# Kernel optimization log

Hardware: AMD Instinct MI355X
Metric: run time of the kernel (lower is better)

## Reference

```python
import jax, jax.numpy as jnp
import numpy as np

N = 10000
F_IN = 512
HID = 256
N_CLS = 64


def setup_inputs() -> dict:
    key = jax.random.key(0)
    k_feat, k_adj, k_w1, k_b1, k_w2, k_b2 = jax.random.split(key, 6)
    feature = jax.random.normal(k_feat, (N, F_IN), dtype=jnp.float32)
    # normalized-adjacency-like dense matrix (sparse-ish values, scaled)
    adj = jax.random.uniform(k_adj, (N, N), dtype=jnp.float32) * (1.0 / N)
    # GCNConv params: glorot-style weights, zero bias
    s1 = 1.0 / np.sqrt(F_IN)
    s2 = 1.0 / np.sqrt(HID)
    W1 = jax.random.uniform(k_w1, (F_IN, HID), jnp.float32, -s1, s1)
    b1 = jnp.zeros((HID,), jnp.float32)
    W2 = jax.random.uniform(k_w2, (HID, N_CLS), jnp.float32, -s2, s2)
    b2 = jnp.zeros((N_CLS,), jnp.float32)
    return {"feature": feature, "adj": adj, "W1": W1, "b1": b1, "W2": W2, "b2": b2}


def gcn_conv(x, adj, W, b):
    # support = x @ W ; out = adj @ support + b
    return adj @ (x @ W) + b


def reference(feature, adj, W1, b1, W2, b2):
    x1 = jax.nn.relu(gcn_conv(feature, adj, W1, b1))
    # dropout is identity in eval mode
    x2 = gcn_conv(x1, adj, W2, b2)
    return (x1, jax.nn.log_softmax(x2, axis=1))
```

## Files before the change

### kernel.cpp

```cpp
#include <hip/hip_runtime.h>
#include <hip/hip_bf16.h>


#define NROW 10000
#define FIN  512
#define HID  256
#define NCLS 64
#define KSPLIT2 4
#define KSPAN2  2560
#define KSPLIT4 8
#define KSPAN4  1280

typedef __bf16 bf8_t __attribute__((ext_vector_type(8)));
typedef __bf16 bf4_t __attribute__((ext_vector_type(4)));
typedef float  f4_t  __attribute__((ext_vector_type(4)));
typedef short  s8_t  __attribute__((ext_vector_type(8)));

__global__ void cvt_f32_bf16(const float* __restrict__ in, __bf16* __restrict__ out, int n) {
    int stride = gridDim.x * blockDim.x * 4;
    for (int i = (blockIdx.x * blockDim.x + threadIdx.x) * 4; i < n; i += stride) {
        f4_t v = *(const f4_t*)(in + i);
        bf4_t o;
        o[0] = (__bf16)v[0]; o[1] = (__bf16)v[1]; o[2] = (__bf16)v[2]; o[3] = (__bf16)v[3];
        *(bf4_t*)(out + i) = o;
    }
}

__global__ void cvt_transpose(const float* __restrict__ in, __bf16* __restrict__ out, int K, int Nn) {
    int idx = blockIdx.x * 256 + threadIdx.x;
    if (idx < K * Nn) {
        int k = idx / Nn, n = idx % Nn;
        out[n * K + k] = (__bf16)in[idx];
    }
}

template<int BM, int BN, int BK, bool AF32, int EPI>
__global__ void __launch_bounds__(256, 4)
gemm_bt(const void* __restrict__ Ap, const __bf16* __restrict__ Bt,
        int M, int Nn, int K, int lda, int ldb, int kspan,
        float* __restrict__ outF, __bf16* __restrict__ outB,
        int ldo, long partStride)
{
    constexpr int WM = BM / 2, WN = BN / 2;
    constexpr int MI = WM / 16, NI = WN / 16;
    constexpr int LDS_K = BK + 8;
    __shared__ __bf16 As[BM * LDS_K];
    __shared__ __bf16 Bs[BN * LDS_K];

    const int tid  = threadIdx.x;
    const int lane = tid & 63;
    const int wave = tid >> 6;
    const int wm = wave >> 1, wn = wave & 1;
    const int m0 = blockIdx.x * BM;
    const int n0 = blockIdx.y * BN;
    const int kbase = blockIdx.z * kspan;
    const int kend  = min(K, kbase + kspan);

    f4_t acc[MI][NI];
    #pragma unroll
    for (int i = 0; i < MI; i++)
        #pragma unroll
        for (int j = 0; j < NI; j++)
            acc[i][j] = f4_t{0.f, 0.f, 0.f, 0.f};

    const int lrow  = lane & 15;
    const int koff0 = (lane >> 4) * 8;

    for (int k0 = kbase; k0 < kend; k0 += BK) {
        if constexpr (AF32) {
            const float* A = (const float*)Ap;
            #pragma unroll
            for (int i = 0; i < BM * BK / 4 / 256; ++i) {
                int idx = tid + i * 256;
                int r = idx / (BK / 4), c = idx % (BK / 4);
                int gm = m0 + r, gk = k0 + c * 4;
                f4_t v = f4_t{0.f, 0.f, 0.f, 0.f};
                if (gm < M && gk < kend) v = *(const f4_t*)(A + (long)gm * lda + gk);
                bf4_t o;
                o[0] = (__bf16)v[0]; o[1] = (__bf16)v[1]; o[2] = (__bf16)v[2]; o[3] = (__bf16)v[3];
                *(bf4_t*)&As[r * LDS_K + c * 4] = o;
            }
        } else {
            const short* A = (const short*)Ap;
            #pragma unroll
            for (int i = 0; i < BM * BK / 8 / 256; ++i) {
                int idx = tid + i * 256;
                int r = idx / (BK / 8), c = idx % (BK / 8);
                int gm = m0 + r, gk = k0 + c * 8;
                s8_t v = s8_t{0,0,0,0,0,0,0,0};
                if (gm < M && gk < kend) v = *(const s8_t*)(A + (long)gm * lda + gk);
                *(s8_t*)&As[r * LDS_K + c * 8] = v;
            }
        }
        {
            const short* B = (const short*)Bt;
            #pragma unroll
            for (int i = 0; i < BN * BK / 8 / 256; ++i) {
                int idx = tid + i * 256;
                int r = idx / (BK / 8), c = idx % (BK / 8);
                int gn = n0 + r, gk = k0 + c * 8;
                s8_t v = s8_t{0,0,0,0,0,0,0,0};
                if (gn < Nn && gk < kend) v = *(const s8_t*)(B + (long)gn * ldb + gk);
                *(s8_t*)&Bs[r * LDS_K + c * 8] = v;
            }
        }
        __syncthreads();
        #pragma unroll
        for (int ks = 0; ks < BK; ks += 32) {
            bf8_t af[MI], bfv[NI];
            #pragma unroll
            for (int mi = 0; mi < MI; mi++)
                af[mi] = *(const bf8_t*)&As[(wm * WM + mi * 16 + lrow) * LDS_K + ks + koff0];
            #pragma unroll
            for (int ni = 0; ni < NI; ni++)
                bfv[ni] = *(const bf8_t*)&Bs[(wn * WN + ni * 16 + lrow) * LDS_K + ks + koff0];
            #pragma unroll
            for (int mi = 0; mi < MI; mi++)
                #pragma unroll
                for (int ni = 0; ni < NI; ni++)
                    acc[mi][ni] = __builtin_amdgcn_mfma_f32_16x16x32_bf16(
                        af[mi], bfv[ni], acc[mi][ni], 0, 0, 0);
        }
        __syncthreads();
    }

    const int erow = wm * WM + (lane >> 4) * 4;
    const int ecol = wn * WN + lrow;
    #pragma unroll
    for (int mi = 0; mi < MI; mi++) {
        #pragma unroll
        for (int ni = 0; ni < NI; ni++) {
            #pragma unroll
            for (int r = 0; r < 4; r++) {
                int grow = m0 + erow + mi * 16 + r;
                int gcol = n0 + ecol + ni * 16;
                if (grow < M && gcol < Nn) {
                    float v = acc[mi][ni][r];
                    if constexpr (EPI == 0) {
                        outB[(long)grow * ldo + gcol] = (__bf16)v;
                    } else {
                        outF[blockIdx.z * partStride + (long)grow * ldo + gcol] = v;
                    }
                }
            }
        }
    }
}

__global__ void relu_bias_fin(const float* __restrict__ part, const float* __restrict__ b1,
                              float* __restrict__ outF, __bf16* __restrict__ outB) {
    long i = (long)(blockIdx.x * 256 + threadIdx.x) * 4;
    f4_t v = *(const f4_t*)(part + i);
    #pragma unroll
    for (int s = 1; s < KSPLIT2; s++) {
        f4_t p = *(const f4_t*)(part + (long)s * NROW * HID + i);
        v[0] += p[0]; v[1] += p[1]; v[2] += p[2]; v[3] += p[3];
    }
    int col = (int)(i & (HID - 1));
    f4_t b = *(const f4_t*)(b1 + col);
    f4_t y;
    bf4_t yb;
    #pragma unroll
    for (int j = 0; j < 4; j++) {
        y[j] = fmaxf(v[j] + b[j], 0.f);
        yb[j] = (__bf16)y[j];
    }
    *(f4_t*)(outF + i) = y;
    *(bf4_t*)(outB + i) = yb;
}

__global__ void logsoftmax_fin(const float* __restrict__ part, const float* __restrict__ b2,
                               float* __restrict__ out, int M) {
    int row  = blockIdx.x * 4 + (threadIdx.x >> 6);
    int lane = threadIdx.x & 63;
    if (row >= M) return;
    float v = b2[lane];
    #pragma unroll
    for (int s = 0; s < KSPLIT4; s++) v += part[((long)s * M + row) * NCLS + lane];
    float m = v;
    #pragma unroll
    for (int off = 32; off > 0; off >>= 1) m = fmaxf(m, __shfl_xor(m, off));
    float e = __expf(v - m);
    float sum = e;
    #pragma unroll
    for (int off = 32; off > 0; off >>= 1) sum += __shfl_xor(sum, off);
    out[(long)row * NCLS + lane] = (v - m) - __logf(sum);
}

extern "C" void kernel_launch(void* const* d_in, const int* in_sizes, int n_in,
                              void* d_out, int out_size, void* d_ws, size_t ws_size,
                              hipStream_t stream) {
    const float* feat = (const float*)d_in[0];
    const float* adj  = (const float*)d_in[1];
    const float* W1   = (const float*)d_in[2];
    const float* b1   = (const float*)d_in[3];
    const float* W2   = (const float*)d_in[4];
    const float* b2   = (const float*)d_in[5];
    float* out = (float*)d_out;
    char* ws = (char*)d_ws;

    __bf16* featb = (__bf16*)(ws);
    __bf16* W1t   = (__bf16*)(ws + 10240000);
    __bf16* W2t   = (__bf16*)(ws + 10502144);
    __bf16* S1t   = (__bf16*)(ws + 10534912);
    __bf16* x1b   = (__bf16*)(ws + 15654912);
    __bf16* S2t   = (__bf16*)(ws + 20774912);
    float*  part  = (float*) (ws + 22054912);

    cvt_f32_bf16<<<640, 256, 0, stream>>>(feat, featb, NROW * FIN);
    cvt_transpose<<<(FIN * HID + 255) / 256, 256, 0, stream>>>(W1, W1t, FIN, HID);
    cvt_transpose<<<(HID * NCLS + 255) / 256, 256, 0, stream>>>(W2, W2t, HID, NCLS);

    gemm_bt<64, 128, 64, false, 0><<<dim3(4, 79, 1), 256, 0, stream>>>(
        W1t, featb, HID, NROW, FIN, FIN, FIN, FIN,
        nullptr, S1t, NROW, 0);

    gemm_bt<64, 128, 64, true, 2><<<dim3(157, 2, KSPLIT2), 256, 0, stream>>>(
        adj, S1t, NROW, HID, NROW, NROW, NROW, KSPAN2,
        part, nullptr, HID, (long)NROW * HID);

    relu_bias_fin<<<NROW * HID / 4 / 256, 256, 0, stream>>>(part, b1, out, x1b);

    gemm_bt<64, 64, 64, false, 0><<<dim3(1, 157, 1), 256, 0, stream>>>(
        W2t, x1b, NCLS, NROW, HID, HID, HID, HID,
        nullptr, S2t, NROW, 0);

    gemm_bt<64, 64, 64, true, 2><<<dim3(157, 1, KSPLIT4), 256, 0, stream>>>(
        adj, S2t, NROW, NCLS, NROW, NROW, NROW, KSPAN4,
        part, nullptr, NCLS, (long)NROW * NCLS);

    logsoftmax_fin<<<2500, 256, 0, stream>>>(part, b2, out + (long)NROW * HID, NROW);
}
```

Before: 886.3 us.

## Prefetch next K-tile into registers while computing current tile in GEMM

Restructures the GEMM main loop so global loads for the next K-tile are issued into registers before the MFMA compute on the current LDS tile. The loaded values are written to LDS at the start of the next iteration. This hides global memory latency behind compute in a software-pipelined way, at the cost of extra registers that may reduce occupancy under the 256x4 launch bounds.

```diff
diff --git a/kernel.cpp b/kernel.cpp
--- a/kernel.cpp
+++ b/kernel.cpp
@@ -44,6 +44,8 @@
     constexpr int WM = BM / 2, WN = BN / 2;
     constexpr int MI = WM / 16, NI = WN / 16;
     constexpr int LDS_K = BK + 8;
+    constexpr int ACH = AF32 ? (BM * BK / 4 / 256) : (BM * BK / 8 / 256);
+    constexpr int BCH = BN * BK / 8 / 256;
     __shared__ __bf16 As[BM * LDS_K];
     __shared__ __bf16 Bs[BN * LDS_K];
 
@@ -66,45 +68,81 @@
     const int lrow  = lane & 15;
     const int koff0 = (lane >> 4) * 8;
 
-    for (int k0 = kbase; k0 < kend; k0 += BK) {
+    f4_t aPreF[AF32 ? ACH : 1];
+    s8_t aPreH[AF32 ? 1 : ACH];
+    s8_t bPre[BCH];
+
+    auto issueA = [&](int k0) {
         if constexpr (AF32) {
             const float* A = (const float*)Ap;
             #pragma unroll
-            for (int i = 0; i < BM * BK / 4 / 256; ++i) {
+            for (int i = 0; i < ACH; ++i) {
                 int idx = tid + i * 256;
                 int r = idx / (BK / 4), c = idx % (BK / 4);
                 int gm = m0 + r, gk = k0 + c * 4;
                 f4_t v = f4_t{0.f, 0.f, 0.f, 0.f};
                 if (gm < M && gk < kend) v = *(const f4_t*)(A + (long)gm * lda + gk);
-                bf4_t o;
-                o[0] = (__bf16)v[0]; o[1] = (__bf16)v[1]; o[2] = (__bf16)v[2]; o[3] = (__bf16)v[3];
-                *(bf4_t*)&As[r * LDS_K + c * 4] = o;
+                aPreF[i] = v;
             }
         } else {
             const short* A = (const short*)Ap;
             #pragma unroll
-            for (int i = 0; i < BM * BK / 8 / 256; ++i) {
+            for (int i = 0; i < ACH; ++i) {
                 int idx = tid + i * 256;
                 int r = idx / (BK / 8), c = idx % (BK / 8);
                 int gm = m0 + r, gk = k0 + c * 8;
                 s8_t v = s8_t{0,0,0,0,0,0,0,0};
                 if (gm < M && gk < kend) v = *(const s8_t*)(A + (long)gm * lda + gk);
-                *(s8_t*)&As[r * LDS_K + c * 8] = v;
-            }
-        }
-        {
-            const short* B = (const short*)Bt;
-            #pragma unroll
-            for (int i = 0; i < BN * BK / 8 / 256; ++i) {
+                aPreH[i] = v;
+            }
+        }
+    };
+    auto issueB = [&](int k0) {
+        const short* B = (const short*)Bt;
+        #pragma unroll
+        for (int i = 0; i < BCH; ++i) {
+            int idx = tid + i * 256;
+            int r = idx / (BK / 8), c = idx % (BK / 8);
+            int gn = n0 + r, gk = k0 + c * 8;
+            s8_t v = s8_t{0,0,0,0,0,0,0,0};
+            if (gn < Nn && gk < kend) v = *(const s8_t*)(B + (long)gn * ldb + gk);
+            bPre[i] = v;
+        }
+    };
+    auto storeAB = [&]() {
+        if constexpr (AF32) {
+            #pragma unroll
+            for (int i = 0; i < ACH; ++i) {
+                int idx = tid + i * 256;
+                int r = idx / (BK / 4), c = idx % (BK / 4);
+                f4_t v = aPreF[i];
+                bf4_t o;
+                o[0] = (__bf16)v[0]; o[1] = (__bf16)v[1]; o[2] = (__bf16)v[2]; o[3] = (__bf16)v[3];
+                *(bf4_t*)&As[r * LDS_K + c * 4] = o;
+            }
+        } else {
+            #pragma unroll
+            for (int i = 0; i < ACH; ++i) {
                 int idx = tid + i * 256;
                 int r = idx / (BK / 8), c = idx % (BK / 8);
-                int gn = n0 + r, gk = k0 + c * 8;
-                s8_t v = s8_t{0,0,0,0,0,0,0,0};
-                if (gn < Nn && gk < kend) v = *(const s8_t*)(B + (long)gn * ldb + gk);
-                *(s8_t*)&Bs[r * LDS_K + c * 8] = v;
-            }
-        }
+                *(s8_t*)&As[r * LDS_K + c * 8] = aPreH[i];
+            }
+        }
+        #pragma unroll
+        for (int i = 0; i < BCH; ++i) {
+            int idx = tid + i * 256;
+            int r = idx / (BK / 8), c = idx % (BK / 8);
+            *(s8_t*)&Bs[r * LDS_K + c * 8] = bPre[i];
+        }
+    };
+
+    issueA(kbase);
+    issueB(kbase);
+    for (int k0 = kbase; k0 < kend; k0 += BK) {
+        storeAB();
         __syncthreads();
+        int kn = k0 + BK;
+        if (kn < kend) { issueA(kn); issueB(kn); }
         #pragma unroll
         for (int ks = 0; ks < BK; ks += 32) {
             bf8_t af[MI], bfv[NI];
```

After: 751.9 us. 15.2% less time.

## Pre-convert adjacency to padded bf16 and prefetch GEMM tiles through registers

Applied to the files above, without the earlier changes.

Adds a kernel that converts the dense adjacency matrix to bf16 once, padded to a K of 10048, so both adjacency GEMMs load bf16 instead of converting f32 per tile. The GEMM loads the next tiles into registers while the current tile is being computed, drops the per-element bounds checks, removes the LDS row padding and relaxes launch bounds to 3 waves. The cost is an extra full pass over the 400MB f32 adjacency, a 200MB bf16 write, and memsets of the padded supports. Without the padding, LDS fragment reads may hit bank conflicts, and the last row tiles read past the logical end of their buffers into other workspace regions.

```diff
diff --git a/kernel.cpp b/kernel.cpp
--- a/kernel.cpp
+++ b/kernel.cpp
@@ -6,6 +6,7 @@
 #define FIN  512
 #define HID  256
 #define NCLS 64
+#define KP   10048
 #define KSPLIT2 4
 #define KSPAN2  2560
 #define KSPLIT4 8
@@ -15,6 +16,21 @@
 typedef __bf16 bf4_t __attribute__((ext_vector_type(4)));
 typedef float  f4_t  __attribute__((ext_vector_type(4)));
 typedef short  s8_t  __attribute__((ext_vector_type(8)));
+
+__global__ void cvt_adj(const float* __restrict__ in, __bf16* __restrict__ out) {
+    int idx = blockIdx.x * 256 + threadIdx.x;
+    if (idx >= KP / 4) return;
+    int r = blockIdx.y;
+    int c0 = idx * 4;
+    bf4_t o;
+    if (c0 + 4 <= NROW) {
+        f4_t v = *(const f4_t*)(in + (long)r * NROW + c0);
+        o[0] = (__bf16)v[0]; o[1] = (__bf16)v[1]; o[2] = (__bf16)v[2]; o[3] = (__bf16)v[3];
+    } else {
+        o[0] = (__bf16)0.f; o[1] = (__bf16)0.f; o[2] = (__bf16)0.f; o[3] = (__bf16)0.f;
+    }
+    *(bf4_t*)(out + (long)r * KP + c0) = o;
+}
 
 __global__ void cvt_f32_bf16(const float* __restrict__ in, __bf16* __restrict__ out, int n) {
     int stride = gridDim.x * blockDim.x * 4;
@@ -34,18 +50,20 @@
     }
 }
 
-template<int BM, int BN, int BK, bool AF32, int EPI>
-__global__ void __launch_bounds__(256, 4)
-gemm_bt(const void* __restrict__ Ap, const __bf16* __restrict__ Bt,
+template<int BM, int BN, int BK, int EPI>
+__global__ void __launch_bounds__(256, 3)
+gemm_bt(const __bf16* __restrict__ A, const __bf16* __restrict__ Bt,
         int M, int Nn, int K, int lda, int ldb, int kspan,
         float* __restrict__ outF, __bf16* __restrict__ outB,
         int ldo, long partStride)
 {
     constexpr int WM = BM / 2, WN = BN / 2;
     constexpr int MI = WM / 16, NI = WN / 16;
-    constexpr int LDS_K = BK + 8;
-    __shared__ __bf16 As[BM * LDS_K];
-    __shared__ __bf16 Bs[BN * LDS_K];
+    constexpr int CPR = BK / 8;
+    constexpr int ACH = BM * BK / 8 / 256;
+    constexpr int BCH = BN * BK / 8 / 256;
+    __shared__ __bf16 As[BM * BK];
+    __shared__ __bf16 Bs[BN * BK];
 
     const int tid  = threadIdx.x;
     const int lane = tid & 63;
@@ -66,54 +84,46 @@
     const int lrow  = lane & 15;
     const int koff0 = (lane >> 4) * 8;
 
-    for (int k0 = kbase; k0 < kend; k0 += BK) {
-        if constexpr (AF32) {
-            const float* A = (const float*)Ap;
-            #pragma unroll
-            for (int i = 0; i < BM * BK / 4 / 256; ++i) {
-                int idx = tid + i * 256;
-                int r = idx / (BK / 4), c = idx % (BK / 4);
-                int gm = m0 + r, gk = k0 + c * 4;
-                f4_t v = f4_t{0.f, 0.f, 0.f, 0.f};
-                if (gm < M && gk < kend) v = *(const f4_t*)(A + (long)gm * lda + gk);
-                bf4_t o;
-                o[0] = (__bf16)v[0]; o[1] = (__bf16)v[1]; o[2] = (__bf16)v[2]; o[3] = (__bf16)v[3];
-                *(bf4_t*)&As[r * LDS_K + c * 4] = o;
-            }
-        } else {
-            const short* A = (const short*)Ap;
-            #pragma unroll
-            for (int i = 0; i < BM * BK / 8 / 256; ++i) {
-                int idx = tid + i * 256;
-                int r = idx / (BK / 8), c = idx % (BK / 8);
-                int gm = m0 + r, gk = k0 + c * 8;
-                s8_t v = s8_t{0,0,0,0,0,0,0,0};
-                if (gm < M && gk < kend) v = *(const s8_t*)(A + (long)gm * lda + gk);
-                *(s8_t*)&As[r * LDS_K + c * 8] = v;
-            }
-        }
-        {
-            const short* B = (const short*)Bt;
-            #pragma unroll
-            for (int i = 0; i < BN * BK / 8 / 256; ++i) {
-                int idx = tid + i * 256;
-                int r = idx / (BK / 8), c = idx % (BK / 8);
-                int gn = n0 + r, gk = k0 + c * 8;
-                s8_t v = s8_t{0,0,0,0,0,0,0,0};
-                if (gn < Nn && gk < kend) v = *(const s8_t*)(B + (long)gn * ldb + gk);
-                *(s8_t*)&Bs[r * LDS_K + c * 8] = v;
-            }
-        }
+    s8_t pA0[ACH], pB0[BCH], pA1[ACH], pB1[BCH];
+
+    auto issueTile = [&](int k0, s8_t* pa, s8_t* pb) {
+        #pragma unroll
+        for (int i = 0; i < ACH; ++i) {
+            int idx = tid + i * 256;
+            pa[i] = *(const s8_t*)(A + (long)(m0 + idx / CPR) * lda + k0 + (idx % CPR) * 8);
+        }
+        #pragma unroll
+        for (int i = 0; i < BCH; ++i) {
+            int idx = tid + i * 256;
+            pb[i] = *(const s8_t*)(Bt + (long)(n0 + idx / CPR) * ldb + k0 + (idx % CPR) * 8);
+        }
+    };
+    auto storeTile = [&](s8_t* pa, s8_t* pb) {
+        #pragma unroll
+        for (int i = 0; i < ACH; ++i) *(s8_t*)&As[(tid + i * 256) * 8] = pa[i];
+        #pragma unroll
+        for (int i = 0; i < BCH; ++i) *(s8_t*)&Bs[(tid + i * 256) * 8] = pb[i];
+    };
+
+    issueTile(kbase, pA0, pB0);
+    issueTile(kbase + BK, pA1, pB1);
+    int it = 0;
+    for (int k0 = kbase; k0 < kend; k0 += BK, ++it) {
+        if ((it & 1) == 0) storeTile(pA0, pB0); else storeTile(pA1, pB1);
         __syncthreads();
+        int kpre = k0 + 2 * BK;
+        if (kpre < kend) {
+            if ((it & 1) == 0) issueTile(kpre, pA0, pB0); else issueTile(kpre, pA1, pB1);
+        }
         #pragma unroll
         for (int ks = 0; ks < BK; ks += 32) {
             bf8_t af[MI], bfv[NI];
             #pragma unroll
             for (int mi = 0; mi < MI; mi++)
-                af[mi] = *(const bf8_t*)&As[(wm * WM + mi * 16 + lrow) * LDS_K + ks + koff0];
+                af[mi] = *(const bf8_t*)&As[(wm * WM + mi * 16 + lrow) * BK + ks + koff0];
             #pragma unroll
             for (int ni = 0; ni < NI; ni++)
-                bfv[ni] = *(const bf8_t*)&Bs[(wn * WN + ni * 16 + lrow) * LDS_K + ks + koff0];
+                bfv[ni] = *(const bf8_t*)&Bs[(wn * WN + ni * 16 + lrow) * BK + ks + koff0];
             #pragma unroll
             for (int mi = 0; mi < MI; mi++)
                 #pragma unroll
@@ -199,34 +209,39 @@
     float* out = (float*)d_out;
     char* ws = (char*)d_ws;
 
-    __bf16* featb = (__bf16*)(ws);
-    __bf16* W1t   = (__bf16*)(ws + 10240000);
-    __bf16* W2t   = (__bf16*)(ws + 10502144);
-    __bf16* S1t   = (__bf16*)(ws + 10534912);
-    __bf16* x1b   = (__bf16*)(ws + 15654912);
-    __bf16* S2t   = (__bf16*)(ws + 20774912);
-    float*  part  = (float*) (ws + 22054912);
-
+    __bf16* adjb  = (__bf16*)(ws);
+    __bf16* featb = (__bf16*)(ws + 201922048);
+    __bf16* W1t   = (__bf16*)(ws + 212211200);
+    __bf16* W2t   = (__bf16*)(ws + 212473344);
+    __bf16* S1t   = (__bf16*)(ws + 212506112);
+    __bf16* x1b   = (__bf16*)(ws + 217650688);
+    __bf16* S2t   = (__bf16*)(ws + 222795264);
+    float*  part  = (float*) (ws + 224081408);
+
+    hipMemsetAsync(S1t, 0, (size_t)HID * KP * 2, stream);
+    hipMemsetAsync(S2t, 0, (size_t)NCLS * KP * 2, stream);
+
+    cvt_adj<<<dim3(10, NROW), 256, 0, stream>>>(adj, adjb);
     cvt_f32_bf16<<<640, 256, 0, stream>>>(feat, featb, NROW * FIN);
     cvt_transpose<<<(FIN * HID + 255) / 256, 256, 0, stream>>>(W1, W1t, FIN, HID);
     cvt_transpose<<<(HID * NCLS + 255) / 256, 256, 0, stream>>>(W2, W2t, HID, NCLS);
 
-    gemm_bt<64, 128, 64, false, 0><<<dim3(4, 79, 1), 256, 0, stream>>>(
+    gemm_bt<64, 64, 64, 0><<<dim3(4, 157, 1), 256, 0, stream>>>(
         W1t, featb, HID, NROW, FIN, FIN, FIN, FIN,
-        nullptr, S1t, NROW, 0);
-
-    gemm_bt<64, 128, 64, true, 2><<<dim3(157, 2, KSPLIT2), 256, 0, stream>>>(
-        adj, S1t, NROW, HID, NROW, NROW, NROW, KSPAN2,
+        nullptr, S1t, KP, 0);
+
+    gemm_bt<64, 128, 64, 2><<<dim3(157, 2, KSPLIT2), 256, 0, stream>>>(
+        adjb, S1t, NROW, HID, KP, KP, KP, KSPAN2,
         part, nullptr, HID, (long)NROW * HID);
 
     relu_bias_fin<<<NROW * HID / 4 / 256, 256, 0, stream>>>(part, b1, out, x1b);
 
-    gemm_bt<64, 64, 64, false, 0><<<dim3(1, 157, 1), 256, 0, stream>>>(
+    gemm_bt<64, 64, 64, 0><<<dim3(1, 157, 1), 256, 0, stream>>>(
         W2t, x1b, NCLS, NROW, HID, HID, HID, HID,
-        nullptr, S2t, NROW, 0);
-
-    gemm_bt<64, 64, 64, true, 2><<<dim3(157, 1, KSPLIT4), 256, 0, stream>>>(
-        adj, S2t, NROW, NCLS, NROW, NROW, NROW, KSPAN4,
+        nullptr, S2t, KP, 0);
+
+    gemm_bt<64, 64, 64, 2><<<dim3(157, 1, KSPLIT4), 256, 0, stream>>>(
+        adjb, S2t, NROW, NCLS, KP, KP, KP, KSPAN4,
         part, nullptr, NCLS, (long)NROW * NCLS);
 
     logsoftmax_fin<<<2500, 256, 0, stream>>>(part, b2, out + (long)NROW * HID, NROW);
```

Measured after the change: 771.9 us. 12.9% less time.

## Load bf16 GEMM tiles via direct global-to-LDS DMA with padded K

Applied to the files above, without the earlier changes.

Replaces register-staged bf16 tile loads with global_load_lds direct-to-LDS transfers, removing LDS padding and the per-element bounds checks. The S1t/S2t intermediates are stored with a padded, zero-filled leading dimension of 10048 so the adjacency GEMMs can read past K without guards, and fp32 adj loads use clamped precomputed row pointers instead of predicates. This adds two memsets and drops LDS padding, which may bring back bank conflicts on the fragment reads.

```diff
diff --git a/kernel.cpp b/kernel.cpp
--- a/kernel.cpp
+++ b/kernel.cpp
@@ -6,6 +6,7 @@
 #define FIN  512
 #define HID  256
 #define NCLS 64
+#define KP   10048
 #define KSPLIT2 4
 #define KSPAN2  2560
 #define KSPLIT4 8
@@ -14,7 +15,13 @@
 typedef __bf16 bf8_t __attribute__((ext_vector_type(8)));
 typedef __bf16 bf4_t __attribute__((ext_vector_type(4)));
 typedef float  f4_t  __attribute__((ext_vector_type(4)));
-typedef short  s8_t  __attribute__((ext_vector_type(8)));
+
+typedef __attribute__((address_space(3))) void       lds_void;
+typedef const __attribute__((address_space(1))) void glb_void;
+
+__device__ __forceinline__ void dma16(const void* g, void* l) {
+    __builtin_amdgcn_global_load_lds((glb_void*)g, (lds_void*)l, 16, 0, 0);
+}
 
 __global__ void cvt_f32_bf16(const float* __restrict__ in, __bf16* __restrict__ out, int n) {
     int stride = gridDim.x * blockDim.x * 4;
@@ -34,18 +41,20 @@
     }
 }
 
-template<int BM, int BN, int BK, bool AF32, int EPI>
+template<int BN, bool AF32, int EPI>
 __global__ void __launch_bounds__(256, 4)
 gemm_bt(const void* __restrict__ Ap, const __bf16* __restrict__ Bt,
-        int M, int Nn, int K, int lda, int ldb, int kspan,
+        int M, int Nn, int K, int Kclamp, int lda, int ldb, int kspan,
         float* __restrict__ outF, __bf16* __restrict__ outB,
         int ldo, long partStride)
 {
+    constexpr int BM = 64, BK = 64;
     constexpr int WM = BM / 2, WN = BN / 2;
     constexpr int MI = WM / 16, NI = WN / 16;
-    constexpr int LDS_K = BK + 8;
-    __shared__ __bf16 As[BM * LDS_K];
-    __shared__ __bf16 Bs[BN * LDS_K];
+    constexpr int BCALLS = BN / 32;
+    constexpr int ACALLS = BM / 32;
+    __shared__ __bf16 As[BM * BK];
+    __shared__ __bf16 Bs[BN * BK];
 
     const int tid  = threadIdx.x;
     const int lane = tid & 63;
@@ -66,54 +75,65 @@
     const int lrow  = lane & 15;
     const int koff0 = (lane >> 4) * 8;
 
+    const __bf16* Brow[BCALLS];
+    #pragma unroll
+    for (int j = 0; j < BCALLS; ++j) {
+        int c = wave + j * 4;
+        Brow[j] = Bt + (long)(n0 + c * 8 + (lane >> 3)) * ldb + (lane & 7) * 8;
+    }
+    const float* Arow[4];
+    int Acol[4], AldsOff[4];
+    const __bf16* ArowB[ACALLS];
+    if constexpr (AF32) {
+        #pragma unroll
+        for (int i = 0; i < 4; ++i) {
+            int idx = tid + i * 256;
+            int r = idx >> 4, c4 = idx & 15;
+            Arow[i] = (const float*)Ap + (long)min(m0 + r, M - 1) * lda;
+            Acol[i] = c4 * 4;
+            AldsOff[i] = r * BK + c4 * 4;
+        }
+    } else {
+        #pragma unroll
+        for (int j = 0; j < ACALLS; ++j) {
+            int c = wave + j * 4;
+            ArowB[j] = (const __bf16*)Ap + (long)(m0 + c * 8 + (lane >> 3)) * lda + (lane & 7) * 8;
+        }
+    }
+
     for (int k0 = kbase; k0 < kend; k0 += BK) {
         if constexpr (AF32) {
-            const float* A = (const float*)Ap;
-            #pragma unroll
-            for (int i = 0; i < BM * BK / 4 / 256; ++i) {
-                int idx = tid + i * 256;
-                int r = idx / (BK / 4), c = idx % (BK / 4);
-                int gm = m0 + r, gk = k0 + c * 4;
-                f4_t v = f4_t{0.f, 0.f, 0.f, 0.f};
-                if (gm < M && gk < kend) v = *(const f4_t*)(A + (long)gm * lda + gk);
+            f4_t av[4];
+            #pragma unroll
+            for (int i = 0; i < 4; ++i)
+                av[i] = *(const f4_t*)(Arow[i] + min(k0 + Acol[i], Kclamp - 4));
+            #pragma unroll
+            for (int i = 0; i < 4; ++i) {
                 bf4_t o;
-                o[0] = (__bf16)v[0]; o[1] = (__bf16)v[1]; o[2] = (__bf16)v[2]; o[3] = (__bf16)v[3];
-                *(bf4_t*)&As[r * LDS_K + c * 4] = o;
+                o[0] = (__bf16)av[i][0]; o[1] = (__bf16)av[i][1];
+                o[2] = (__bf16)av[i][2]; o[3] = (__bf16)av[i][3];
+                *(bf4_t*)&As[AldsOff[i]] = o;
             }
         } else {
-            const short* A = (const short*)Ap;
-            #pragma unroll
-            for (int i = 0; i < BM * BK / 8 / 256; ++i) {
-                int idx = tid + i * 256;
-                int r = idx / (BK / 8), c = idx % (BK / 8);
-                int gm = m0 + r, gk = k0 + c * 8;
-                s8_t v = s8_t{0,0,0,0,0,0,0,0};
-                if (gm < M && gk < kend) v = *(const s8_t*)(A + (long)gm * lda + gk);
-                *(s8_t*)&As[r * LDS_K + c * 8] = v;
-            }
-        }
-        {
-            const short* B = (const short*)Bt;
-            #pragma unroll
-            for (int i = 0; i < BN * BK / 8 / 256; ++i) {
-                int idx = tid + i * 256;
-                int r = idx / (BK / 8), c = idx % (BK / 8);
-                int gn = n0 + r, gk = k0 + c * 8;
-                s8_t v = s8_t{0,0,0,0,0,0,0,0};
-                if (gn < Nn && gk < kend) v = *(const s8_t*)(B + (long)gn * ldb + gk);
-                *(s8_t*)&Bs[r * LDS_K + c * 8] = v;
-            }
-        }
+            #pragma unroll
+            for (int j = 0; j < ACALLS; ++j)
+                dma16(ArowB[j] + k0, &As[(wave + j * 4) * 512]);
+        }
+        #pragma unroll
+        for (int j = 0; j < BCALLS; ++j)
+            dma16(Brow[j] + k0, &Bs[(wave + j * 4) * 512]);
+
         __syncthreads();
+
         #pragma unroll
         for (int ks = 0; ks < BK; ks += 32) {
             bf8_t af[MI], bfv[NI];
             #pragma unroll
             for (int mi = 0; mi < MI; mi++)
-                af[mi] = *(const bf8_t*)&As[(wm * WM + mi * 16 + lrow) * LDS_K + ks + koff0];
+                af[mi] = *(const bf8_t*)&As[(wm * WM + mi * 16 + lrow) * BK + ks + koff0];
             #pragma unroll
             for (int ni = 0; ni < NI; ni++)
-                bfv[ni] = *(const bf8_t*)&Bs[(wn * WN + ni * 16 + lrow) * LDS_K + ks + koff0];
+                bfv[ni] = *(const bf8_t*)&Bs[(wn * WN + ni * 16 + lrow) * BK + ks + koff0];
             #pragma unroll
             for (int mi = 0; mi < MI; mi++)
                 #pragma unroll
@@ -200,33 +220,36 @@
     char* ws = (char*)d_ws;
 
     __bf16* featb = (__bf16*)(ws);
-    __bf16* W1t   = (__bf16*)(ws + 10240000);
-    __bf16* W2t   = (__bf16*)(ws + 10502144);
-    __bf16* S1t   = (__bf16*)(ws + 10534912);
-    __bf16* x1b   = (__bf16*)(ws + 15654912);
-    __bf16* S2t   = (__bf16*)(ws + 20774912);
-    float*  part  = (float*) (ws + 22054912);
+    __bf16* W1t   = (__bf16*)(ws + 10289152);
+    __bf16* W2t   = (__bf16*)(ws + 10551296);
+    __bf16* S1t   = (__bf16*)(ws + 10584064);
+    __bf16* x1b   = (__bf16*)(ws + 15728640);
+    __bf16* S2t   = (__bf16*)(ws + 20873216);
+    float*  part  = (float*) (ws + 22159360);
+
+    hipMemsetAsync(S1t, 0, (size_t)HID * KP * 2, stream);
+    hipMemsetAsync(S2t, 0, (size_t)NCLS * KP * 2, stream);
 
     cvt_f32_bf16<<<640, 256, 0, stream>>>(feat, featb, NROW * FIN);
     cvt_transpose<<<(FIN * HID + 255) / 256, 256, 0, stream>>>(W1, W1t, FIN, HID);
     cvt_transpose<<<(HID * NCLS + 255) / 256, 256, 0, stream>>>(W2, W2t, HID, NCLS);
 
-    gemm_bt<64, 128, 64, false, 0><<<dim3(4, 79, 1), 256, 0, stream>>>(
-        W1t, featb, HID, NROW, FIN, FIN, FIN, FIN,
-        nullptr, S1t, NROW, 0);
-
-    gemm_bt<64, 128, 64, true, 2><<<dim3(157, 2, KSPLIT2), 256, 0, stream>>>(
-        adj, S1t, NROW, HID, NROW, NROW, NROW, KSPAN2,
+    gemm_bt<64, false, 0><<<dim3(4, 157, 1), 256, 0, stream>>>(
+        W1t, featb, HID, NROW, FIN, FIN, FIN, FIN, FIN,
+        nullptr, S1t, KP, 0);
+
+    gemm_bt<128, true, 2><<<dim3(157, 2, KSPLIT2), 256, 0, stream>>>(
+        adj, S1t, NROW, HID, KP, NROW, NROW, KP, KSPAN2,
         part, nullptr, HID, (long)NROW * HID);
 
     relu_bias_fin<<<NROW * HID / 4 / 256, 256, 0, stream>>>(part, b1, out, x1b);
 
-    gemm_bt<64, 64, 64, false, 0><<<dim3(1, 157, 1), 256, 0, stream>>>(
-        W2t, x1b, NCLS, NROW, HID, HID, HID, HID,
-        nullptr, S2t, NROW, 0);
-
-    gemm_bt<64, 64, 64, true, 2><<<dim3(157, 1, KSPLIT4), 256, 0, stream>>>(
-        adj, S2t, NROW, NCLS, NROW, NROW, NROW, KSPAN4,
+    gemm_bt<64, false, 0><<<dim3(1, 157, 1), 256, 0, stream>>>(
+        W2t, x1b, NCLS, NROW, HID, HID, HID, HID, HID,
+        nullptr, S2t, KP, 0);
+
+    gemm_bt<64, true, 2><<<dim3(157, 1, KSPLIT4), 256, 0, stream>>>(
+        adj, S2t, NROW, NCLS, KP, NROW, NROW, KP, KSPAN4,
         part, nullptr, NCLS, (long)NROW * NCLS);
 
     logsoftmax_fin<<<2500, 256, 0, stream>>>(part, b2, out + (long)NROW * HID, NROW);
```

Measured after the change: 730.0 us. -17.6%, faster.
